# Kernel optimization log

Hardware: AMD Instinct MI355X
Metric: run time of the kernel (lower is better)

## Reference

```python
import jax, jax.numpy as jnp
import numpy as np

EPS = 1e-5
NEG = -1e9

def rmsnorm(x, g, eps=EPS):
    x32 = x.astype(jnp.float32)
    n = x32 * jax.lax.rsqrt(jnp.mean(x32 * x32, axis=-1, keepdims=True) + eps)
    return g * n.astype(x.dtype)

def setup_inputs() -> dict:
    key = jax.random.key(0)
    ks = jax.random.split(key, 10)
    B, S, D, H = 2, 2048, 768, 12
    F = 4 * D
    s = 0.02
    return {
        "x": jax.random.normal(ks[0], (B, S, D), jnp.float32),
        "mask": jax.random.randint(ks[1], (B, S, S), 0, 2, jnp.int32),
        "wq": jax.random.normal(ks[2], (D, D), jnp.float32) * s,
        "wk": jax.random.normal(ks[3], (D, D), jnp.float32) * s,
        "wv": jax.random.normal(ks[4], (D, D), jnp.float32) * s,
        "wo": jax.random.normal(ks[5], (D, D), jnp.float32) * s,
        "w1": jax.random.normal(ks[6], (F, D), jnp.float32) * s,
        "w2": jax.random.normal(ks[7], (D, F), jnp.float32) * s,
        "w3": jax.random.normal(ks[8], (F, D), jnp.float32) * s,
        "g_attn": jnp.ones((D,), jnp.float32),
        "g_ffn": jnp.ones((D,), jnp.float32),
    }

def reference(x, mask, wq, wk, wv, wo, w1, w2, w3, g_attn, g_ffn):
    B, S, D = x.shape
    H = 12
    Dk = D // H
    # --- attention sub-block (pre-norm) ---
    xn = rmsnorm(x, g_attn)
    # torch Linear: y = x @ W^T; split heads -> [B,H,S,Dk]
    q = (xn @ wq.T).reshape(B, S, H, Dk).transpose(0, 2, 1, 3)
    k = (xn @ wk.T).reshape(B, S, H, Dk).transpose(0, 2, 1, 3)
    v = (xn @ wv.T).reshape(B, S, H, Dk).transpose(0, 2, 1, 3)
    scores = jnp.einsum("bhqd,bhkd->bhqk", q, k) / jnp.sqrt(jnp.float32(Dk))
    scores = jnp.where(mask[:, None, :, :] == 0, jnp.float32(NEG), scores)
    probs = jax.nn.softmax(scores, axis=-1)  # dropout p=0.0 -> identity
    attn = jnp.einsum("bhqk,bhkd->bhqd", probs, v)
    attn = attn.transpose(0, 2, 1, 3).reshape(B, S, D)
    h = x + attn @ wo.T
    # --- SwiGLU FFN sub-block (pre-norm) ---
    hn = rmsnorm(h, g_ffn)
    ffn = (jax.nn.silu(hn @ w1.T) * (hn @ w3.T)) @ w2.T
    return h + ffn
```

## Files before the change

### kernel.cpp

```cpp
#include <hip/hip_runtime.h>
#include <hip/hip_bf16.h>

#define S_LEN 2048
#define D_MODEL 768
#define NH 12
#define DK 64
#define F_DIM 3072
#define BATCH 2
#define M_ROWS (BATCH * S_LEN)

typedef __bf16 bf16x8 __attribute__((ext_vector_type(8)));
typedef float floatx4 __attribute__((ext_vector_type(4)));
typedef unsigned short u16;
typedef unsigned long long u64;

__device__ inline float bf2f(u16 u) {
    union { unsigned int i; float f; } x; x.i = ((unsigned int)u) << 16; return x.f;
}
__device__ inline u16 f2bf(float f) {
    union { float f; unsigned int i; } x; x.f = f;
    unsigned int r = x.i + 0x7fffu + ((x.i >> 16) & 1u);
    return (u16)(r >> 16);
}
__device__ __forceinline__ bf16x8 as_bf16x8(uint4 v) {
    union { uint4 u; bf16x8 b; } c; c.u = v; return c.b;
}

__device__ __forceinline__ void ldsload16(const u16* g, u16* l) {
    __builtin_amdgcn_global_load_lds(
        (const __attribute__((address_space(1))) unsigned int*)g,
        (__attribute__((address_space(3))) unsigned int*)l, 16, 0, 0);
}

__device__ __forceinline__ void cvt_body(
        int i,
        const float4* wq, const float4* wk, const float4* wv, const float4* wo,
        const float4* w1, const float4* w2, const float4* w3,
        ushort4* wqkvf, ushort4* wob, ushort4* w13f, ushort4* w2b) {
    const int WS4 = (D_MODEL * D_MODEL) / 4;
    const int WB4 = (F_DIM * D_MODEL) / 4;
    const int RW4 = D_MODEL / 4;
    const float4* src; ushort4* dst; int off, doff;
    if (i < 4 * WS4) {
        int s = i / WS4; off = i - s * WS4;
        src = (s == 0) ? wq : (s == 1) ? wk : (s == 2) ? wv : wo;
        if (s == 3) { dst = wob; doff = off; }
        else {
            dst = wqkvf;
            int row = off / RW4, c4 = off - row * RW4;
            int k = c4 * 4;
            int rg = s * D_MODEL + row;
            int n_tile = rg >> 4, nl = rg & 15;
            int k_tile = k >> 5, qd = (k >> 3) & 3, jj = k & 7;
            int ln = qd * 16 + nl;
            int f = n_tile * 24 + k_tile;
            doff = (f * 512 + ln * 8 + jj) >> 2;
        }
    } else {
        int j = i - 4 * WS4; int s = j / WB4; off = j - s * WB4;
        if (s == 1) { src = w2; dst = w2b; doff = off; }
        else {
            src = (s == 0) ? w1 : w3;
            dst = w13f;
            int which = (s == 0) ? 0 : 1;
            int row = off / RW4, c4 = off - row * RW4;
            int k = c4 * 4;
            int n_tile = row >> 4, nl = row & 15;
            int k_tile = k >> 5, qd = (k >> 3) & 3, jj = k & 7;
            int ln = qd * 16 + nl;
            int f = (n_tile * 24 + k_tile) * 2 + which;
            doff = (f * 512 + ln * 8 + jj) >> 2;
        }
    }
    float4 v = src[off];
    ushort4 o;
    o.x = f2bf(v.x); o.y = f2bf(v.y); o.z = f2bf(v.z); o.w = f2bf(v.w);
    dst[doff] = o;
}

__device__ __forceinline__ void mask_body(int bx, const int* m, u64* bits) {
    size_t base = (size_t)bx * 2048 + threadIdx.x;
    #pragma unroll
    for (int it = 0; it < 8; ++it) {
        size_t gid = base + (size_t)it * 256;
        u64 b = __ballot(m[gid] != 0);
        if ((threadIdx.x & 63) == 0) bits[gid >> 6] = b;
    }
}

__device__ __forceinline__ void rms_body(int row, const float* x, const float* g,
                                         u16* out, float* red) {
    const float* xr = x + (size_t)row * D_MODEL;
    u16* orow = out + (size_t)row * D_MODEL;
    int t = threadIdx.x;
    float v0 = xr[t];
    float v1 = xr[t + 256];
    float v2 = xr[t + 512];
    float ss = v0 * v0 + v1 * v1 + v2 * v2;
    #pragma unroll
    for (int off = 1; off < 64; off <<= 1) ss += __shfl_xor(ss, off);
    if ((t & 63) == 0) red[t >> 6] = ss;
    __syncthreads();
    float tot = red[0] + red[1] + red[2] + red[3];
    float scale = rsqrtf(tot * (1.0f / (float)D_MODEL) + 1e-5f);
    orow[t]       = f2bf(g[t]       * v0 * scale);
    orow[t + 256] = f2bf(g[t + 256] * v1 * scale);
    orow[t + 512] = f2bf(g[t + 512] * v2 * scale);
}

__global__ __launch_bounds__(256)
void prep(const float4* wq, const float4* wk, const float4* wv, const float4* wo,
          const float4* w1, const float4* w2, const float4* w3,
          ushort4* wqkvf, ushort4* wob, ushort4* w13f, ushort4* w2b,
          const int* m, u64* bits,
          const float* x, const float* g, u16* xn) {
    __shared__ float red[4];
    int bx = blockIdx.x;
    if (bx < 9216) {
        cvt_body(bx * 256 + threadIdx.x, wq, wk, wv, wo, w1, w2, w3,
                 wqkvf, wob, w13f, w2b);
    } else if (bx < 13312) {
        mask_body(bx - 9216, m, bits);
    } else {
        rms_body(bx - 13312, x, g, xn, red);
    }
}

__global__ __launch_bounds__(256)
void rmsnorm_k(const float* __restrict__ x, const float* __restrict__ g, u16* __restrict__ out) {
    __shared__ float red[4];
    rms_body(blockIdx.x, x, g, out, red);
}

__global__ __launch_bounds__(256, 3)
void gemm_f1(const u16* __restrict__ A, const u16* __restrict__ W13f,
             u16* __restrict__ Cout) {
    const int K = D_MODEL, N = F_DIM;
    __shared__ u16 As[2][64][64];

    int t = threadIdx.x;
    int w = t >> 6, lane = t & 63;
    int lrow = lane & 15, quad = lane >> 4;

    int lid = blockIdx.y * 24 + blockIdx.x;
    int xcd = lid & 7, s = lid >> 3;
    int nb = xcd * 3 + (s % 3);
    int mb = s / 3;
    int mBase = mb * 64;
    int ntile0 = nb * 8 + w * 2;

    int srow8 = lane >> 3;
    int sc64 = ((lane & 7) ^ srow8) * 8;
    const u16* Ag = A + (size_t)(mBase + w * 16 + srow8) * K + sc64;
    const uint4* Bf = (const uint4*)W13f;

    auto stageA = [&](int k0, int b) {
        ldsload16(Ag + k0,                 &As[b][w * 16][0]);
        ldsload16(Ag + (size_t)8 * K + k0, &As[b][w * 16 + 8][0]);
    };

    floatx4 zero = {0.f, 0.f, 0.f, 0.f};
    floatx4 acc[4][2], acc2[4][2];
    #pragma unroll
    for (int r = 0; r < 4; ++r)
        #pragma unroll
        for (int c = 0; c < 2; ++c) { acc[r][c] = zero; acc2[r][c] = zero; }

    stageA(0, 0);
    int cur = 0;
    for (int kt2 = 0; kt2 < 12; ++kt2) {
        uint4 b1v[2][2], b3v[2][2];
        #pragma unroll
        for (int hh = 0; hh < 2; ++hh) {
            int kt = kt2 * 2 + hh;
            #pragma unroll
            for (int c = 0; c < 2; ++c) {
                int f = ((ntile0 + c) * 24 + kt) * 2;
                b1v[hh][c] = Bf[(size_t)f * 64 + lane];
                b3v[hh][c] = Bf[(size_t)(f + 1) * 64 + lane];
            }
        }
        __syncthreads();
        if (kt2 + 1 < 12) stageA((kt2 + 1) * 64, cur ^ 1);

        #pragma unroll
        for (int hh = 0; hh < 2; ++hh) {
            int rc = ((hh * 4 + quad) ^ (lrow & 7)) * 8;
            bf16x8 af[4];
            #pragma unroll
            for (int r = 0; r < 4; ++r) af[r] = *(const bf16x8*)&As[cur][r * 16 + lrow][rc];
            #pragma unroll
            for (int c = 0; c < 2; ++c) {
                bf16x8 b1f = as_bf16x8(b1v[hh][c]);
                bf16x8 b3f = as_bf16x8(b3v[hh][c]);
                #pragma unroll
                for (int r = 0; r < 4; ++r) {
                    acc[r][c]  = __builtin_amdgcn_mfma_f32_16x16x32_bf16(af[r], b1f, acc[r][c], 0, 0, 0);
                    acc2[r][c] = __builtin_amdgcn_mfma_f32_16x16x32_bf16(af[r], b3f, acc2[r][c], 0, 0, 0);
                }
            }
        }
        cur ^= 1;
    }

    #pragma unroll
    for (int r = 0; r < 4; ++r) {
        #pragma unroll
        for (int c = 0; c < 2; ++c) {
            #pragma unroll
            for (int j = 0; j < 4; ++j) {
                int grow = mBase + r * 16 + quad * 4 + j;
                int gcol = nb * 128 + w * 32 + c * 16 + lrow;
                float a = acc[r][c][j];
                Cout[(size_t)grow * N + gcol] = f2bf((a / (1.0f + __expf(-a))) * acc2[r][c][j]);
            }
        }
    }
}

__global__ __launch_bounds__(256, 3)
void gemm64(const u16* __restrict__ A, const u16* __restrict__ B1,
            const float* __restrict__ R, float* __restrict__ Cout, int N, int K) {
    __shared__ u16 As[2][64][64];
    __shared__ u16 Bs[2][64][64];

    int t = threadIdx.x;
    int w = t >> 6, lane = t & 63;

    int L = blockIdx.y * gridDim.x + blockIdx.x;
    int xcd = L & 7;
    int i = L >> 3;
    int mPer = gridDim.y >> 3;
    int nIdx = i / mPer;
    int mIdx = xcd * mPer + i % mPer;
    int mBase = mIdx * 64, nBase = nIdx * 64;

    int lrow = lane & 15, quad = lane >> 4;
    int wm = (w >> 1) * 32, wn = (w & 1) * 32;

    int srow8 = lane >> 3;
    int sc64 = ((lane & 7) ^ srow8) * 8;
    const u16* Ag = A  + (size_t)(mBase + w * 16 + srow8) * K + sc64;
    const u16* Bg = B1 + (size_t)(nBase + w * 16 + srow8) * K + sc64;

    auto stage = [&](int k0, int b) {
        ldsload16(Ag + k0,                 &As[b][w * 16][0]);
        ldsload16(Ag + (size_t)8 * K + k0, &As[b][w * 16 + 8][0]);
        ldsload16(Bg + k0,                 &Bs[b][w * 16][0]);
        ldsload16(Bg + (size_t)8 * K + k0, &Bs[b][w * 16 + 8][0]);
    };

    floatx4 zero = {0.f, 0.f, 0.f, 0.f};
    floatx4 acc[2][2];
    #pragma unroll
    for (int r = 0; r < 2; ++r)
        #pragma unroll
        for (int c = 0; c < 2; ++c) acc[r][c] = zero;

    stage(0, 0);
    int cur = 0;
    for (int k0 = 0; k0 < K; k0 += 64) {
        __syncthreads();
        if (k0 + 64 < K) stage(k0 + 64, cur ^ 1);

        #pragma unroll
        for (int half = 0; half < 2; ++half) {
            int rc = ((half * 4 + quad) ^ (lrow & 7)) * 8;
            bf16x8 af[2], bf[2];
            #pragma unroll
            for (int r = 0; r < 2; ++r) af[r] = *(const bf16x8*)&As[cur][wm + r * 16 + lrow][rc];
            #pragma unroll
            for (int c = 0; c < 2; ++c) bf[c] = *(const bf16x8*)&Bs[cur][wn + c * 16 + lrow][rc];
            #pragma unroll
            for (int r = 0; r < 2; ++r)
                #pragma unroll
                for (int c = 0; c < 2; ++c)
                    acc[r][c] = __builtin_amdgcn_mfma_f32_16x16x32_bf16(af[r], bf[c], acc[r][c], 0, 0, 0);
        }
        cur ^= 1;
    }

    #pragma unroll
    for (int r = 0; r < 2; ++r) {
        #pragma unroll
        for (int c = 0; c < 2; ++c) {
            #pragma unroll
            for (int j = 0; j < 4; ++j) {
                int grow = mBase + wm + r * 16 + quad * 4 + j;
                int gcol = nBase + wn + c * 16 + lrow;
                size_t idx = (size_t)grow * N + gcol;
                Cout[idx] = acc[r][c][j] + R[idx];
            }
        }
    }
}

__global__ __launch_bounds__(256, 4)
void gemm_qkv(const u16* __restrict__ A, const u16* __restrict__ Wf,
              u16* __restrict__ qb, u16* __restrict__ kb, u16* __restrict__ vt) {
    const int K = D_MODEL;
    __shared__ u16 As[2][64][64];

    int t = threadIdx.x;
    int w = t >> 6, lane = t & 63;
    int lrow = lane & 15, quad = lane >> 4;

    int L = blockIdx.y * 18 + blockIdx.x;
    int g = (L & 7) * 144 + (L >> 3);
    int nb = g >> 6;
    int mBase = (g & 63) * 64;
    int ntile0 = nb * 8 + w * 2;

    int srow8 = lane >> 3;
    int sc64 = ((lane & 7) ^ srow8) * 8;
    const u16* Ag = A + (size_t)(mBase + w * 16 + srow8) * K + sc64;
    const uint4* Bf = (const uint4*)Wf;

    auto stageA = [&](int k0, int b) {
        ldsload16(Ag + k0,                 &As[b][w * 16][0]);
        ldsload16(Ag + (size_t)8 * K + k0, &As[b][w * 16 + 8][0]);
    };

    floatx4 zero = {0.f, 0.f, 0.f, 0.f};
    floatx4 acc[4][2];
    #pragma unroll
    for (int r = 0; r < 4; ++r)
        #pragma unroll
        for (int c = 0; c < 2; ++c) acc[r][c] = zero;

    stageA(0, 0);
    int cur = 0;
    for (int kt2 = 0; kt2 < 12; ++kt2) {
        uint4 bv[2][2];
        #pragma unroll
        for (int hh = 0; hh < 2; ++hh) {
            int kt = kt2 * 2 + hh;
            #pragma unroll
            for (int c = 0; c < 2; ++c) {
                int f = (ntile0 + c) * 24 + kt;
                bv[hh][c] = Bf[(size_t)f * 64 + lane];
            }
        }
        __syncthreads();
        if (kt2 + 1 < 12) stageA((kt2 + 1) * 64, cur ^ 1);

        #pragma unroll
        for (int hh = 0; hh < 2; ++hh) {
            int rc = ((hh * 4 + quad) ^ (lrow & 7)) * 8;
            bf16x8 af[4];
            #pragma unroll
            for (int r = 0; r < 4; ++r) af[r] = *(const bf16x8*)&As[cur][r * 16 + lrow][rc];
            #pragma unroll
            for (int c = 0; c < 2; ++c) {
                bf16x8 bfr = as_bf16x8(bv[hh][c]);
                #pragma unroll
                for (int r = 0; r < 4; ++r)
                    acc[r][c] = __builtin_amdgcn_mfma_f32_16x16x32_bf16(af[r], bfr, acc[r][c], 0, 0, 0);
            }
        }
        cur ^= 1;
    }

    const float qscale = 0.18033688011112042f;
    int which = nb / 6;
    if (which == 2) {
        __syncthreads();
        u16* T = &As[0][0][0];
        #pragma unroll
        for (int r = 0; r < 4; ++r)
            #pragma unroll
            for (int c = 0; c < 2; ++c) {
                int d = w * 32 + c * 16 + lrow;
                int sc = (d & 7) << 3;
                #pragma unroll
                for (int j = 0; j < 4; ++j) {
                    int s = r * 16 + quad * 4 + j;
                    T[d * 64 + (s ^ sc)] = f2bf(acc[r][c][j]);
                }
            }
        int bb = mBase >> 11, sbase = mBase & 2047;
        #pragma unroll
        for (int i = 0; i < 32; ++i) {
            int dl = w * 32 + i;
            u16 v = T[dl * 64 + (lane ^ ((dl & 7) << 3))];
            int cm = nb * 128 + dl - 2 * D_MODEL;
            int hh = cm >> 6, dd = cm & 63;
            vt[((((size_t)bb * NH + hh) * DK + dd) << 11) + sbase + lane] = v;
        }
    } else {
        u16* dst = (which == 0) ? qb : kb;
        #pragma unroll
        for (int r = 0; r < 4; ++r) {
            #pragma unroll
            for (int c = 0; c < 2; ++c) {
                #pragma unroll
                for (int j = 0; j < 4; ++j) {
                    int grow = mBase + r * 16 + quad * 4 + j;
                    int gcol = nb * 128 + w * 32 + c * 16 + lrow;
                    int cm = gcol - which * D_MODEL;
                    float val = acc[r][c][j];
                    if (which == 0) val *= qscale;
                    dst[(size_t)grow * D_MODEL + cm] = f2bf(val);
                }
            }
        }
    }
}

__global__ __launch_bounds__(256)
void attn_mfma(const u16* __restrict__ q, const u16* __restrict__ k,
               const u16* __restrict__ vt, const u64* __restrict__ mbits,
               u16* __restrict__ out) {
    __shared__ u16 Ks0[2][64][32], Ks1[2][64][32];
    __shared__ u16 Vs0[2][64][32], Vs1[2][64][32];
    __shared__ u16 PT[4][16][64];

    int t = threadIdx.x;
    int lane = t & 63;
    int w = t >> 6;
    int lrow = lane & 15;
    int quad = lane >> 4;

    int L = blockIdx.y * gridDim.x + blockIdx.x;
    int g = (L & 7) * 96 + (L >> 3);
    int st0 = (g & 31) * 64;
    int bh = g >> 5;
    int h = bh % NH;
    int b = bh / NH;

    const u16* kbase = k + (size_t)b * S_LEN * D_MODEL + h * DK;
    const u16* vbase = vt + (size_t)bh * DK * S_LEN;
    const u64* bw = mbits + ((size_t)b * S_LEN + st0 + w * 16 + lrow) * (S_LEN / 64);

    int srow = lane >> 2;
    int scolS = ((lane & 3) ^ ((lane >> 3) & 3)) * 8;
    int rq = (quad ^ ((lrow >> 1) & 3)) * 8;
    int ptw = lrow & 7;
    int rp0 = (quad ^ ptw) * 8;
    int rp1 = ((4 + quad) ^ ptw) * 8;
    int pqo = (quad & 1) * 4;
    int pch = quad >> 1;

    const u16* kg = kbase + (size_t)(w * 16 + srow) * D_MODEL + scolS;
    const u16* vg = vbase + (size_t)(w * 16 + srow) * S_LEN + scolS;

    auto stageKV = [&](int kt, int bsel) {
        ldsload16(kg + (size_t)kt * D_MODEL,      &Ks0[bsel][w * 16][0]);
        ldsload16(kg + (size_t)kt * D_MODEL + 32, &Ks1[bsel][w * 16][0]);
        ldsload16(vg + kt,      &Vs0[bsel][w * 16][0]);
        ldsload16(vg + kt + 32, &Vs1[bsel][w * 16][0]);
    };

    stageKV(0, 0);

    bf16x8 bq0, bq1;
    {
        const u16* qrow = q + ((size_t)b * S_LEN + st0 + w * 16 + lrow) * D_MODEL + h * DK + quad * 8;
        bq0 = *(const bf16x8*)qrow;
        bq1 = *(const bf16x8*)(qrow + 32);
    }

    bf16x8 ones;
    {
        union { u16 u; __bf16 b; } o; o.u = 0x3F80;
        #pragma unroll
        for (int j = 0; j < 8; ++j) ones[j] = o.b;
    }

    floatx4 zero = {0.f, 0.f, 0.f, 0.f};
    floatx4 Ot[4] = {zero, zero, zero, zero};
    floatx4 Osum = zero;

    u64 mw = bw[0];
    __syncthreads();

    int cur = 0;
    for (int kt = 0; kt < S_LEN; kt += 64) {
        if (kt + 64 < S_LEN) stageKV(kt + 64, cur ^ 1);
        u64 mw_next = (kt + 64 < S_LEN) ? bw[(kt >> 6) + 1] : 0ull;
        unsigned mlo = (unsigned)mw, mhi = (unsigned)(mw >> 32);

        floatx4 st[4];
        #pragma unroll
        for (int nt = 0; nt < 4; ++nt) {
            bf16x8 ak0 = *(const bf16x8*)&Ks0[cur][nt * 16 + lrow][rq];
            bf16x8 ak1 = *(const bf16x8*)&Ks1[cur][nt * 16 + lrow][rq];
            st[nt] = __builtin_amdgcn_mfma_f32_16x16x32_bf16(ak0, bq0, zero, 0, 0, 0);
            st[nt] = __builtin_amdgcn_mfma_f32_16x16x32_bf16(ak1, bq1, st[nt], 0, 0, 0);
        }

        #pragma unroll
        for (int nt = 0; nt < 4; ++nt) {
            unsigned half = (nt & 2) ? mhi : mlo;
            unsigned tmp = half >> ((nt & 1) * 16 + quad * 4);
            unsigned eu[4];
            #pragma unroll
            for (int j = 0; j < 4; ++j) {
                float e = __builtin_amdgcn_exp2f(st[nt][j]);
                unsigned msk = (unsigned)((int)(tmp << (31 - j)) >> 31);
                eu[j] = __float_as_uint(e) & msk;
            }
            uint2 p;
            p.x = (eu[0] >> 16) | (eu[1] & 0xffff0000u);
            p.y = (eu[2] >> 16) | (eu[3] & 0xffff0000u);
            int pc = ((nt * 2 + pch) ^ ptw) * 8 + pqo;
            *(uint2*)&PT[w][lrow][pc] = p;
        }

        bf16x8 ap0 = *(const bf16x8*)&PT[w][lrow][rp0];
        bf16x8 ap1 = *(const bf16x8*)&PT[w][lrow][rp1];
        Osum = __builtin_amdgcn_mfma_f32_16x16x32_bf16(ap0, ones, Osum, 0, 0, 0);
        Osum = __builtin_amdgcn_mfma_f32_16x16x32_bf16(ap1, ones, Osum, 0, 0, 0);
        #pragma unroll
        for (int dt = 0; dt < 4; ++dt) {
            bf16x8 bv0 = *(const bf16x8*)&Vs0[cur][dt * 16 + lrow][rq];
            bf16x8 bv1 = *(const bf16x8*)&Vs1[cur][dt * 16 + lrow][rq];
            Ot[dt] = __builtin_amdgcn_mfma_f32_16x16x32_bf16(ap0, bv0, Ot[dt], 0, 0, 0);
            Ot[dt] = __builtin_amdgcn_mfma_f32_16x16x32_bf16(ap1, bv1, Ot[dt], 0, 0, 0);
        }

        __syncthreads();
        cur ^= 1;
        mw = mw_next;
    }

    float invj[4];
    #pragma unroll
    for (int j = 0; j < 4; ++j) invj[j] = 1.0f / Osum[j];

    u16* obase = out + ((size_t)b * S_LEN + st0 + w * 16) * D_MODEL + h * DK;
    #pragma unroll
    for (int dt = 0; dt < 4; ++dt)
        #pragma unroll
        for (int j = 0; j < 4; ++j)
            obase[(size_t)(quad * 4 + j) * D_MODEL + dt * 16 + lrow] = f2bf(Ot[dt][j] * invj[j]);
}

extern "C" void kernel_launch(void* const* d_in, const int* in_sizes, int n_in,
                              void* d_out, int out_size, void* d_ws, size_t ws_size,
                              hipStream_t stream) {
    const float* x      = (const float*)d_in[0];
    const int*   mask   = (const int*)d_in[1];
    const float* wq     = (const float*)d_in[2];
    const float* wk     = (const float*)d_in[3];
    const float* wv     = (const float*)d_in[4];
    const float* wo     = (const float*)d_in[5];
    const float* w1     = (const float*)d_in[6];
    const float* w2     = (const float*)d_in[7];
    const float* w3     = (const float*)d_in[8];
    const float* g_attn = (const float*)d_in[9];
    const float* g_ffn  = (const float*)d_in[10];
    float* out = (float*)d_out;

    const size_t WSMALL = (size_t)D_MODEL * D_MODEL;
    const size_t WBIG   = (size_t)F_DIM * D_MODEL;
    const size_t MD     = (size_t)M_ROWS * D_MODEL;

    char* ws = (char*)d_ws;
    u16* wqkvf = (u16*)ws;           ws += WSMALL * 3 * 2;
    u16* wob  = (u16*)ws;            ws += WSMALL * 2;
    u16* w13f = (u16*)ws;            ws += WBIG * 2 * 2;
    u16* w2b  = (u16*)ws;            ws += WBIG * 2;
    u16* xn  = (u16*)ws;             ws += MD * 2;
    u16* qb  = (u16*)ws;             ws += MD * 2;
    u16* kb  = (u16*)ws;             ws += MD * 2;
    u16* vb  = (u16*)ws;             ws += MD * 2;
    u16* ao  = (u16*)ws;             ws += MD * 2;
    float* hb = (float*)ws;          ws += MD * 4;
    u64* mb  = (u64*)ws;             ws += (size_t)BATCH * S_LEN * (S_LEN / 64) * 8;
    u16* hn = xn;
    u16* ub = qb;
    (void)ws_size; (void)n_in; (void)in_sizes; (void)out_size;

    dim3 blk(256);

    prep<<<17408, blk, 0, stream>>>((const float4*)wq, (const float4*)wk, (const float4*)wv,
                                    (const float4*)wo, (const float4*)w1, (const float4*)w2,
                                    (const float4*)w3,
                                    (ushort4*)wqkvf, (ushort4*)wob, (ushort4*)w13f, (ushort4*)w2b,
                                    mask, mb, x, g_attn, xn);

    gemm_qkv<<<dim3(18, M_ROWS / 64), blk, 0, stream>>>(xn, wqkvf, qb, kb, vb);
    attn_mfma<<<dim3(S_LEN / 64, BATCH * NH), blk, 0, stream>>>(qb, kb, vb, mb, ao);
    gemm64<<<dim3(D_MODEL / 64, M_ROWS / 64), blk, 0, stream>>>(ao, wob, x, hb, D_MODEL, D_MODEL);
    rmsnorm_k<<<M_ROWS, blk, 0, stream>>>((const float*)hb, g_ffn, hn);
    gemm_f1<<<dim3(24, M_ROWS / 64), blk, 0, stream>>>(hn, w13f, ub);
    gemm64<<<dim3(D_MODEL / 64, M_ROWS / 64), blk, 0, stream>>>(ub, w2b, hb, out, D_MODEL, F_DIM);
}
```

Baseline: 309.1 us.

## Split attention key range in two halves with a separate combine kernel

The attention kernel now splits the key dimension into two halves, doubling the grid from 768 to 1536 blocks. Each block writes unnormalized fp32 partial outputs and row sums, and a new combine kernel adds the two halves, normalizes and writes the bf16 output. This targets low occupancy, since 768 blocks on 256 CUs leaves each block running a long serial loop. In exchange it adds an extra launch and fp32 partial traffic, and reuses the hb and out buffers as scratch for the partials.

New measurement: 318.1 us. +2.9%, slower.

```diff
diff --git a/kernel.cpp b/kernel.cpp
--- a/kernel.cpp
+++ b/kernel.cpp
@@ -410,7 +410,8 @@
 __global__ __launch_bounds__(256)
 void attn_mfma(const u16* __restrict__ q, const u16* __restrict__ k,
                const u16* __restrict__ vt, const u64* __restrict__ mbits,
-               u16* __restrict__ out) {
+               float* __restrict__ po0, float* __restrict__ po1,
+               float* __restrict__ ps) {
     __shared__ u16 Ks0[2][64][32], Ks1[2][64][32];
     __shared__ u16 Vs0[2][64][32], Vs1[2][64][32];
     __shared__ u16 PT[4][16][64];
@@ -422,11 +423,15 @@
     int quad = lane >> 4;
 
     int L = blockIdx.y * gridDim.x + blockIdx.x;
-    int g = (L & 7) * 96 + (L >> 3);
+    int g = (L & 7) * 192 + (L >> 3);
     int st0 = (g & 31) * 64;
-    int bh = g >> 5;
+    int combo = g >> 5;
+    int half = combo & 1;
+    int bh = combo >> 1;
     int h = bh % NH;
     int b = bh / NH;
+    int kt0 = half * (S_LEN / 2);
+    int kt_end = kt0 + (S_LEN / 2);
 
     const u16* kbase = k + (size_t)b * S_LEN * D_MODEL + h * DK;
     const u16* vbase = vt + (size_t)bh * DK * S_LEN;
@@ -451,7 +456,7 @@
         ldsload16(vg + kt + 32, &Vs1[bsel][w * 16][0]);
     };
 
-    stageKV(0, 0);
+    stageKV(kt0, 0);
 
     bf16x8 bq0, bq1;
     {
@@ -471,13 +476,13 @@
     floatx4 Ot[4] = {zero, zero, zero, zero};
     floatx4 Osum = zero;
 
-    u64 mw = bw[0];
+    u64 mw = bw[kt0 >> 6];
     __syncthreads();
 
     int cur = 0;
-    for (int kt = 0; kt < S_LEN; kt += 64) {
-        if (kt + 64 < S_LEN) stageKV(kt + 64, cur ^ 1);
-        u64 mw_next = (kt + 64 < S_LEN) ? bw[(kt >> 6) + 1] : 0ull;
+    for (int kt = kt0; kt < kt_end; kt += 64) {
+        if (kt + 64 < kt_end) stageKV(kt + 64, cur ^ 1);
+        u64 mw_next = (kt + 64 < kt_end) ? bw[(kt >> 6) + 1] : 0ull;
         unsigned mlo = (unsigned)mw, mhi = (unsigned)(mw >> 32);
 
         floatx4 st[4];
@@ -491,8 +496,8 @@
 
         #pragma unroll
         for (int nt = 0; nt < 4; ++nt) {
-            unsigned half = (nt & 2) ? mhi : mlo;
-            unsigned tmp = half >> ((nt & 1) * 16 + quad * 4);
+            unsigned half2 = (nt & 2) ? mhi : mlo;
+            unsigned tmp = half2 >> ((nt & 1) * 16 + quad * 4);
             unsigned eu[4];
             #pragma unroll
             for (int j = 0; j < 4; ++j) {
@@ -524,16 +529,41 @@
         mw = mw_next;
     }
 
-    float invj[4];
-    #pragma unroll
-    for (int j = 0; j < 4; ++j) invj[j] = 1.0f / Osum[j];
-
-    u16* obase = out + ((size_t)b * S_LEN + st0 + w * 16) * D_MODEL + h * DK;
+    float* po = half ? po1 : po0;
+    float* ob = po + ((size_t)bh * S_LEN + st0 + w * 16) * DK;
     #pragma unroll
     for (int dt = 0; dt < 4; ++dt)
         #pragma unroll
         for (int j = 0; j < 4; ++j)
-            obase[(size_t)(quad * 4 + j) * D_MODEL + dt * 16 + lrow] = f2bf(Ot[dt][j] * invj[j]);
+            ob[(size_t)(quad * 4 + j) * DK + dt * 16 + lrow] = Ot[dt][j];
+    if (lrow == 0) {
+        float* psh = ps + (size_t)half * (BATCH * NH * S_LEN)
+                        + (size_t)bh * S_LEN + st0 + w * 16;
+        #pragma unroll
+        for (int j = 0; j < 4; ++j) psh[quad * 4 + j] = Osum[j];
+    }
+}
+
+__global__ __launch_bounds__(256)
+void attn_combine(const float* __restrict__ po0, const float* __restrict__ po1,
+                  const float* __restrict__ ps, u16* __restrict__ ao) {
+    int idx = blockIdx.x * 256 + threadIdx.x;
+    int row = idx / 192;
+    int c4 = (idx - row * 192) * 4;
+    int b = row >> 11, s = row & 2047;
+    int h = c4 >> 6, d = c4 & 63;
+    int bh = b * NH + h;
+    size_t pb = ((size_t)bh * S_LEN + s) * DK + d;
+    float4 a0 = *(const float4*)(po0 + pb);
+    float4 a1 = *(const float4*)(po1 + pb);
+    float inv = 1.0f / (ps[(size_t)bh * S_LEN + s]
+                      + ps[(size_t)BATCH * NH * S_LEN + (size_t)bh * S_LEN + s]);
+    ushort4 o;
+    o.x = f2bf((a0.x + a1.x) * inv);
+    o.y = f2bf((a0.y + a1.y) * inv);
+    o.z = f2bf((a0.z + a1.z) * inv);
+    o.w = f2bf((a0.w + a1.w) * inv);
+    *(ushort4*)(ao + (size_t)row * D_MODEL + c4) = o;
 }
 
 extern "C" void kernel_launch(void* const* d_in, const int* in_sizes, int n_in,
@@ -568,8 +598,11 @@
     u16* ao  = (u16*)ws;             ws += MD * 2;
     float* hb = (float*)ws;          ws += MD * 4;
     u64* mb  = (u64*)ws;             ws += (size_t)BATCH * S_LEN * (S_LEN / 64) * 8;
+    float* psum = (float*)ws;        ws += (size_t)2 * BATCH * NH * S_LEN * 4;
     u16* hn = xn;
     u16* ub = qb;
+    float* po0 = hb;
+    float* po1 = out;
     (void)ws_size; (void)n_in; (void)in_sizes; (void)out_size;
 
     dim3 blk(256);
@@ -581,7 +614,8 @@
                                     mask, mb, x, g_attn, xn);
 
     gemm_qkv<<<dim3(18, M_ROWS / 64), blk, 0, stream>>>(xn, wqkvf, qb, kb, vb);
-    attn_mfma<<<dim3(S_LEN / 64, BATCH * NH), blk, 0, stream>>>(qb, kb, vb, mb, ao);
+    attn_mfma<<<dim3(32, 48), blk, 0, stream>>>(qb, kb, vb, mb, po0, po1, psum);
+    attn_combine<<<(M_ROWS * D_MODEL) / 1024, blk, 0, stream>>>(po0, po1, psum, ao);
     gemm64<<<dim3(D_MODEL / 64, M_ROWS / 64), blk, 0, stream>>>(ao, wob, x, hb, D_MODEL, D_MODEL);
     rmsnorm_k<<<M_ROWS, blk, 0, stream>>>((const float*)hb, g_ffn, hn);
     gemm_f1<<<dim3(24, M_ROWS / 64), blk, 0, stream>>>(hn, w13f, ub);
```
